# Kernel optimization log

Hardware: AMD Instinct MI355X
Metric: run time of the kernel (lower is better)

## Reference

```python
import jax, jax.numpy as jnp
import numpy as np

N = 50000
E = 1600000
D_IN = 128
D_OUT = 128


def setup_inputs() -> dict:
    key = jax.random.key(0)
    k1, k2, k3, k4, k5, k6 = jax.random.split(key, 6)
    row = jax.random.randint(k1, (E,), 0, N, dtype=jnp.int32)
    col = jax.random.randint(k2, (E,), 0, N, dtype=jnp.int32)
    vals = jax.random.uniform(k3, (E,), dtype=jnp.float32)
    features = jax.random.normal(k4, (N, D_IN), dtype=jnp.float32)
    weight = jax.random.normal(k5, (D_IN, D_OUT), dtype=jnp.float32)
    bias = jax.random.normal(k6, (D_OUT,), dtype=jnp.float32)
    return {"row": row, "col": col, "vals": vals, "features": features,
            "weight": weight, "bias": bias}


def reference(row, col, vals, features, weight, bias):
    # SpMM aggregation: out[i] = sum_j adj[i,j] * features[j]
    # adj given in COO: (row, col, vals)
    gathered = vals[:, None] * features[col]          # [E, D_IN]
    agg = jax.ops.segment_sum(gathered, row, num_segments=N)  # [N, D_IN]
    # dense feature transform + bias
    return agg @ weight + bias                        # [N, D_OUT]
```

## Files before the change

kernel.cpp:

```cpp
#include <hip/hip_runtime.h>
#include <hip/hip_bf16.h>


#define D 128
#define NREP 8
#define RPB 128
#define BCAP 5120
#define EPB 4096
#define NBMAX 512

typedef __attribute__((ext_vector_type(8))) short short8;
typedef __attribute__((ext_vector_type(4))) float f32x4;

__device__ __forceinline__ ushort bf16bits(float x) {
    return __hip_bfloat16_raw(__float2bfloat16(x)).x;
}

__global__ __launch_bounds__(256) void prep_k(const float* __restrict__ W,
                                              ushort* __restrict__ Wt,
                                              int* __restrict__ gcur, int NB) {
    const int idx = blockIdx.x * 256 + threadIdx.x;
    if (idx < D * D) {
        const int k = idx >> 7, c = idx & 127;
        Wt[c * D + k] = bf16bits(W[idx]);
    }
    if (idx < NB) gcur[idx] = 0;
}

__global__ __launch_bounds__(256) void fused_gemm_scatter_k(
    const float* __restrict__ F, const ushort* __restrict__ Wt,
    ushort* __restrict__ Gb, int nrows,
    const int* __restrict__ row, const int* __restrict__ col,
    const float* __restrict__ vals, int* __restrict__ gcur,
    uint2* __restrict__ pairs, int E, int NB, int SB) {
    __shared__ int hist[NBMAX];
    __shared__ int cur[NBMAX];

    if ((int)blockIdx.x >= SB) {
        const int gb = (int)blockIdx.x - SB;
        const int wave = threadIdx.x >> 6;
        const int lane = threadIdx.x & 63;
        const int r0 = (gb * 8 + wave * 2) * 16;
        if (r0 >= nrows) return;
        const int lr = lane & 15;
        const int lg = lane >> 4;

        f32x4 acc0[8], acc1[8];
        #pragma unroll
        for (int c = 0; c < 8; ++c) {
            acc0[c] = (f32x4){0.f, 0.f, 0.f, 0.f};
            acc1[c] = (f32x4){0.f, 0.f, 0.f, 0.f};
        }

        int ar0 = r0 + lr;      if (ar0 >= nrows) ar0 = nrows - 1;
        int ar1 = r0 + 16 + lr; if (ar1 >= nrows) ar1 = nrows - 1;
        const float* __restrict__ a0p = F + (size_t)ar0 * D + lg * 8;
        const float* __restrict__ a1p = F + (size_t)ar1 * D + lg * 8;

        #pragma unroll
        for (int kk = 0; kk < 4; ++kk) {
            const float4 x0 = *(const float4*)(a0p + kk * 32);
            const float4 x1 = *(const float4*)(a0p + kk * 32 + 4);
            const float4 y0 = *(const float4*)(a1p + kk * 32);
            const float4 y1 = *(const float4*)(a1p + kk * 32 + 4);
            short8 af0, af1;
            af0[0] = (short)bf16bits(x0.x); af0[1] = (short)bf16bits(x0.y);
            af0[2] = (short)bf16bits(x0.z); af0[3] = (short)bf16bits(x0.w);
            af0[4] = (short)bf16bits(x1.x); af0[5] = (short)bf16bits(x1.y);
            af0[6] = (short)bf16bits(x1.z); af0[7] = (short)bf16bits(x1.w);
            af1[0] = (short)bf16bits(y0.x); af1[1] = (short)bf16bits(y0.y);
            af1[2] = (short)bf16bits(y0.z); af1[3] = (short)bf16bits(y0.w);
            af1[4] = (short)bf16bits(y1.x); af1[5] = (short)bf16bits(y1.y);
            af1[6] = (short)bf16bits(y1.z); af1[7] = (short)bf16bits(y1.w);
            #pragma unroll
            for (int c = 0; c < 8; ++c) {
                const short8 bf = *(const short8*)(Wt + (size_t)(c * 16 + lr) * D + kk * 32 + lg * 8);
                acc0[c] = __builtin_amdgcn_mfma_f32_16x16x32_bf16(af0, bf, acc0[c], 0, 0, 0);
                acc1[c] = __builtin_amdgcn_mfma_f32_16x16x32_bf16(af1, bf, acc1[c], 0, 0, 0);
            }
        }

        uint* __restrict__ g32 = (uint*)Gb;
        #pragma unroll
        for (int i = 0; i < 4; ++i) {
            const int rr0 = r0 + 4 * lg + i;
            if (rr0 < nrows) {
                #pragma unroll
                for (int c = 0; c < 4; ++c)
                    g32[(size_t)rr0 * 64 + c * 16 + lr] =
                        (uint)bf16bits(acc0[c][i]) | ((uint)bf16bits(acc0[c + 4][i]) << 16);
            }
            const int rr1 = r0 + 16 + 4 * lg + i;
            if (rr1 < nrows) {
                #pragma unroll
                for (int c = 0; c < 4; ++c)
                    g32[(size_t)rr1 * 64 + c * 16 + lr] =
                        (uint)bf16bits(acc1[c][i]) | ((uint)bf16bits(acc1[c + 4][i]) << 16);
            }
        }
        return;
    }

    const int t = threadIdx.x;
    for (int i = t; i < NB; i += 256) hist[i] = 0;
    __syncthreads();

    const int e0 = (int)blockIdx.x * EPB;
    const int e1 = min(e0 + EPB, E);

    for (int e = e0 + t; e < e1; e += 512) {
        const int ra = row[e];
        const bool has2 = (e + 256 < e1);
        const int rb = has2 ? row[e + 256] : 0;
        atomicAdd(&hist[ra >> 7], 1);
        if (has2) atomicAdd(&hist[rb >> 7], 1);
    }
    __syncthreads();

    for (int i = t; i < NB; i += 256) {
        const int h = hist[i];
        cur[i] = (h > 0) ? atomicAdd(&gcur[i], h) : 0;
    }
    __syncthreads();

    for (int e = e0 + t; e < e1; e += 512) {
        const int ra = row[e];
        const int ca = col[e];
        const float va = vals[e];
        const bool has2 = (e + 256 < e1);
        int rb = 0, cb = 0;
        float vb = 0.f;
        if (has2) { rb = row[e + 256]; cb = col[e + 256]; vb = vals[e + 256]; }
        const int ba = ra >> 7;
        const int sa = atomicAdd(&cur[ba], 1);
        if (sa < BCAP)
            pairs[(size_t)ba * BCAP + sa] =
                make_uint2(((uint)ca << 16) | bf16bits(va), (uint)(ra & (RPB - 1)));
        if (has2) {
            const int bb = rb >> 7;
            const int sb = atomicAdd(&cur[bb], 1);
            if (sb < BCAP)
                pairs[(size_t)bb * BCAP + sb] =
                    make_uint2(((uint)cb << 16) | bf16bits(vb), (uint)(rb & (RPB - 1)));
        }
    }
}

__global__ __launch_bounds__(1024) void bucket_to_csr_k(
    uint2* __restrict__ bpairs, const int* __restrict__ gcur,
    int* __restrict__ offs, int* __restrict__ counts, int N) {
    __shared__ uint2 ents[BCAP];
    __shared__ int hist[RPB];
    __shared__ int roff[RPB];
    __shared__ int cur[RPB];
    const int t = threadIdx.x, b = blockIdx.x;
    if (t < RPB) hist[t] = 0;
    __syncthreads();

    int cnt = gcur[b];
    if (cnt > BCAP) cnt = BCAP;
    const uint2* __restrict__ in = bpairs + (size_t)b * BCAP;
    for (int j = t; j < cnt; j += 1024) {
        const uint2 e = in[j];
        ents[j] = e;
        atomicAdd(&hist[e.y], 1);
    }
    __syncthreads();

    if (t < RPB) roff[t] = hist[t];
    __syncthreads();
    for (int off = 1; off < RPB; off <<= 1) {
        const int x = (t < RPB && t >= off) ? roff[t - off] : 0;
        __syncthreads();
        if (t < RPB) roff[t] += x;
        __syncthreads();
    }
    if (t < RPB) {
        const int ex = roff[t] - hist[t];
        roff[t] = ex;
        cur[t] = 0;
        const int rg = b * RPB + t;
        if (rg < N) {
            offs[rg] = b * 2 * BCAP + ex;
            counts[rg] = hist[t];
        }
    }
    __syncthreads();

    uint* __restrict__ outv = (uint*)bpairs + (size_t)b * 2 * BCAP;
    for (int j = t; j < cnt; j += 1024) {
        const uint2 e = ents[j];
        const int k = atomicAdd(&cur[e.y], 1);
        outv[roff[e.y] + k] = e.x;
    }
}

__global__ __launch_bounds__(256) void csr_gather_bf16_k(
    const uint* __restrict__ pairs, const int* __restrict__ offs,
    const int* __restrict__ counts, const uint* __restrict__ Gu,
    const float* __restrict__ bias, float* __restrict__ out, int n) {
    const int wid = (blockIdx.x * 256 + threadIdx.x) >> 6;
    if (wid >= n) return;
    const int lane = threadIdx.x & 63;

    float2 acc = make_float2(bias[lane], bias[64 + lane]);
    const int start = offs[wid];
    const int cnt = counts[wid];
    const uint* __restrict__ pp = pairs + start;

    int j = 0;
    for (; j + 15 < cnt; j += 16) {
        uint p[16], g[16];
        #pragma unroll
        for (int k = 0; k < 16; ++k) p[k] = pp[j + k];
        #pragma unroll
        for (int k = 0; k < 16; ++k) g[k] = Gu[(size_t)(p[k] >> 16) * (D / 2) + lane];
        #pragma unroll
        for (int k = 0; k < 16; ++k) {
            const float v = __uint_as_float(p[k] << 16);
            acc.x += v * __uint_as_float(g[k] << 16);
            acc.y += v * __uint_as_float(g[k] & 0xffff0000u);
        }
    }
    for (; j + 3 < cnt; j += 4) {
        uint p[4], g[4];
        #pragma unroll
        for (int k = 0; k < 4; ++k) p[k] = pp[j + k];
        #pragma unroll
        for (int k = 0; k < 4; ++k) g[k] = Gu[(size_t)(p[k] >> 16) * (D / 2) + lane];
        #pragma unroll
        for (int k = 0; k < 4; ++k) {
            const float v = __uint_as_float(p[k] << 16);
            acc.x += v * __uint_as_float(g[k] << 16);
            acc.y += v * __uint_as_float(g[k] & 0xffff0000u);
        }
    }
    for (; j < cnt; ++j) {
        const uint p = pp[j];
        const uint g = Gu[(size_t)(p >> 16) * (D / 2) + lane];
        const float v = __uint_as_float(p << 16);
        acc.x += v * __uint_as_float(g << 16);
        acc.y += v * __uint_as_float(g & 0xffff0000u);
    }
    out[(size_t)wid * D + lane] = acc.x;
    out[(size_t)wid * D + 64 + lane] = acc.y;
}

__global__ __launch_bounds__(256) void transposeW_k(const float* __restrict__ W,
                                                    ushort* __restrict__ Wt) {
    const int idx = blockIdx.x * 256 + threadIdx.x;
    const int k = idx >> 7, c = idx & 127;
    Wt[c * D + k] = bf16bits(W[idx]);
}

__global__ __launch_bounds__(256) void gemm_mfma_k(
    const float* __restrict__ F, const ushort* __restrict__ Wt,
    ushort* __restrict__ Gb, int nrows) {
    const int wave = threadIdx.x >> 6;
    const int lane = threadIdx.x & 63;
    const int row0 = (blockIdx.x * 4 + wave) * 16;
    if (row0 >= nrows) return;
    const int lr = lane & 15;
    const int lg = lane >> 4;

    f32x4 acc[8];
    #pragma unroll
    for (int c = 0; c < 8; ++c) acc[c] = (f32x4){0.f, 0.f, 0.f, 0.f};

    int arow_idx = row0 + lr;
    if (arow_idx >= nrows) arow_idx = nrows - 1;
    const float* __restrict__ arow = F + (size_t)arow_idx * D + lg * 8;

    #pragma unroll
    for (int kk = 0; kk < 4; ++kk) {
        const float4 a0 = *(const float4*)(arow + kk * 32);
        const float4 a1 = *(const float4*)(arow + kk * 32 + 4);
        short8 af;
        af[0] = (short)bf16bits(a0.x); af[1] = (short)bf16bits(a0.y);
        af[2] = (short)bf16bits(a0.z); af[3] = (short)bf16bits(a0.w);
        af[4] = (short)bf16bits(a1.x); af[5] = (short)bf16bits(a1.y);
        af[6] = (short)bf16bits(a1.z); af[7] = (short)bf16bits(a1.w);
        #pragma unroll
        for (int c = 0; c < 8; ++c) {
            const short8 bf = *(const short8*)(Wt + (size_t)(c * 16 + lr) * D + kk * 32 + lg * 8);
            acc[c] = __builtin_amdgcn_mfma_f32_16x16x32_bf16(af, bf, acc[c], 0, 0, 0);
        }
    }

    ushort* __restrict__ gout = Gb + (size_t)row0 * D;
    #pragma unroll
    for (int i = 0; i < 4; ++i) {
        const int r = 4 * lg + i;
        if (row0 + r < nrows) {
            #pragma unroll
            for (int c = 0; c < 8; ++c) {
                const int j = c * 16 + lr;
                const int pos = (c < 4) ? (2 * j) : (2 * (j - 64) + 1);
                gout[(size_t)r * D + pos] = bf16bits(acc[c][i]);
            }
        }
    }
}

__global__ __launch_bounds__(256) void hist_rank_rep_k(const int* __restrict__ row,
                                                       int* __restrict__ cntrep,
                                                       ushort* __restrict__ rank,
                                                       int E, int N) {
    const int e = blockIdx.x * 256 + threadIdx.x;
    if (e >= E) return;
    const int rep = blockIdx.x & (NREP - 1);
    rank[e] = (ushort)atomicAdd(&cntrep[rep * N + row[e]], 1);
}

__global__ __launch_bounds__(256) void repbase_k(int* __restrict__ cntrep,
                                                 int* __restrict__ tot, int N) {
    const int r = blockIdx.x * 256 + threadIdx.x;
    if (r >= N) return;
    int s = 0;
    #pragma unroll
    for (int rep = 0; rep < NREP; ++rep) {
        const int v = cntrep[rep * N + r];
        cntrep[rep * N + r] = s;
        s += v;
    }
    tot[r] = s;
}

__global__ __launch_bounds__(256) void scan_blocks_k(const int* __restrict__ counts,
                                                     int* __restrict__ offs,
                                                     int* __restrict__ blockSums, int n) {
    __shared__ int s[256];
    const int t = threadIdx.x;
    const int i = blockIdx.x * 256 + t;
    const int v = (i < n) ? counts[i] : 0;
    s[t] = v;
    __syncthreads();
    for (int off = 1; off < 256; off <<= 1) {
        int x = (t >= off) ? s[t - off] : 0;
        __syncthreads();
        s[t] += x;
        __syncthreads();
    }
    if (i < n) offs[i] = s[t] - v;
    if (t == 255) blockSums[blockIdx.x] = s[255];
}

__global__ __launch_bounds__(256) void scan_top_k(int* __restrict__ blockSums, int nb) {
    __shared__ int s[256];
    const int t = threadIdx.x;
    const int v = (t < nb) ? blockSums[t] : 0;
    s[t] = v;
    __syncthreads();
    for (int off = 1; off < 256; off <<= 1) {
        int x = (t >= off) ? s[t - off] : 0;
        __syncthreads();
        s[t] += x;
        __syncthreads();
    }
    if (t < nb) blockSums[t] = s[t] - v;
}

__global__ __launch_bounds__(256) void scan_add_k(int* __restrict__ offs,
                                                  const int* __restrict__ blockSums,
                                                  int n) {
    int i = blockIdx.x * 256 + threadIdx.x;
    if (i < n) offs[i] += blockSums[blockIdx.x];
}

__global__ __launch_bounds__(256) void fill_pack_k(const int* __restrict__ row,
                                                   const int* __restrict__ col,
                                                   const float* __restrict__ vals,
                                                   const int* __restrict__ offs,
                                                   const ushort* __restrict__ rank,
                                                   const int* __restrict__ cntrep,
                                                   uint* __restrict__ pairs, int E, int N) {
    const int e = blockIdx.x * 256 + threadIdx.x;
    if (e >= E) return;
    const int r = row[e];
    const int rep = (e >> 8) & (NREP - 1);
    const int pos = offs[r] + cntrep[rep * N + r] + (int)rank[e];
    pairs[pos] = ((uint)col[e] << 16) | bf16bits(vals[e]);
}

#define ROWS_PER_BLOCK 64
__global__ __launch_bounds__(256) void gemm_f32_k(
    const float* __restrict__ A, const float* __restrict__ W,
    const float* __restrict__ bias, float* __restrict__ out, int nrows) {
    __shared__ float Wlds[D * D];
    {
        const float4* W4 = (const float4*)W;
        float4* Wl4 = (float4*)Wlds;
        #pragma unroll
        for (int i = 0; i < (D * D / 4) / 256; ++i)
            Wl4[threadIdx.x + i * 256] = W4[threadIdx.x + i * 256];
    }
    __syncthreads();
    const int lane = threadIdx.x & 31;
    const int rsub = threadIdx.x >> 5;
    const float4 b = ((const float4*)bias)[lane];
    const int rowBase = blockIdx.x * ROWS_PER_BLOCK;
    for (int rr = rsub; rr < ROWS_PER_BLOCK; rr += 8) {
        const int r = rowBase + rr;
        if (r >= nrows) break;
        const float* __restrict__ arow = A + (size_t)r * D;
        float4 acc = b;
        #pragma unroll 4
        for (int k4 = 0; k4 < D / 4; ++k4) {
            const float4 a = ((const float4*)arow)[k4];
            const int k = k4 * 4;
            const float4 w0 = ((const float4*)(Wlds + (k + 0) * D))[lane];
            const float4 w1 = ((const float4*)(Wlds + (k + 1) * D))[lane];
            const float4 w2 = ((const float4*)(Wlds + (k + 2) * D))[lane];
            const float4 w3 = ((const float4*)(Wlds + (k + 3) * D))[lane];
            acc.x += a.x * w0.x + a.y * w1.x + a.z * w2.x + a.w * w3.x;
            acc.y += a.x * w0.y + a.y * w1.y + a.z * w2.y + a.w * w3.y;
            acc.z += a.x * w0.z + a.y * w1.z + a.z * w2.z + a.w * w3.z;
            acc.w += a.x * w0.w + a.y * w1.w + a.z * w2.w + a.w * w3.w;
        }
        ((float4*)(out + (size_t)r * D))[lane] = acc;
    }
}

__global__ __launch_bounds__(256) void spmm_scatter(
    const int* __restrict__ row, const int* __restrict__ col,
    const float* __restrict__ vals, const float* __restrict__ feat,
    float* __restrict__ agg, int E) {
    int gid = blockIdx.x * 256 + threadIdx.x;
    int e = gid >> 5;
    if (e >= E) return;
    int lane = gid & 31;
    int r = row[e];
    int c = col[e];
    float v = vals[e];
    float4 f = ((const float4*)(feat + (size_t)c * D))[lane];
    float* dst = agg + (size_t)r * D + lane * 4;
    atomicAdd(dst + 0, v * f.x);
    atomicAdd(dst + 1, v * f.y);
    atomicAdd(dst + 2, v * f.z);
    atomicAdd(dst + 3, v * f.w);
}

extern "C" void kernel_launch(void* const* d_in, const int* in_sizes, int n_in,
                              void* d_out, int out_size, void* d_ws, size_t ws_size,
                              hipStream_t stream) {
    const int* row = (const int*)d_in[0];
    const int* col = (const int*)d_in[1];
    const float* vals = (const float*)d_in[2];
    const float* feat = (const float*)d_in[3];
    const float* W = (const float*)d_in[4];
    const float* bias = (const float*)d_in[5];
    float* out = (float*)d_out;

    const int E = in_sizes[0];
    const int N = out_size / D;
    const int NB = (N + RPB - 1) / RPB;

    const size_t Gb_bytes = (size_t)N * D * sizeof(ushort);
    const size_t wt_bytes = (size_t)D * D * sizeof(ushort);
    const size_t cnt_bytes = (size_t)N * sizeof(int);

    const size_t bpairs_bytes = (size_t)NB * BCAP * sizeof(uint2);
    const size_t gcur_bytes = ((size_t)NB * sizeof(int) + 255) & ~(size_t)255;
    const size_t need_bucket = Gb_bytes + bpairs_bytes + gcur_bytes +
                               2 * cnt_bytes + wt_bytes;

    const size_t pairs_bytes = (size_t)E * sizeof(uint);
    const size_t rank_bytes = ((size_t)E * sizeof(ushort) + 3) & ~(size_t)3;
    const size_t cntrep_bytes = (size_t)NREP * N * sizeof(int);
    const size_t bs_bytes = 256 * sizeof(int);
    const size_t need_compact = Gb_bytes + pairs_bytes + rank_bytes + cntrep_bytes +
                                2 * cnt_bytes + bs_bytes + wt_bytes;

    if (ws_size >= need_bucket && N <= 65536 && NB <= NBMAX) {
        char* p = (char*)d_ws;
        ushort* Gb = (ushort*)p;   p += Gb_bytes;
        uint2* bpairs = (uint2*)p; p += bpairs_bytes;
        int* gcur = (int*)p;       p += gcur_bytes;
        int* offs = (int*)p;       p += cnt_bytes;
        int* counts = (int*)p;     p += cnt_bytes;
        ushort* Wt = (ushort*)p;   p += wt_bytes;

        const int GB = (N + 127) / 128;
        const int SB = (E + EPB - 1) / EPB;

        prep_k<<<(D * D + 255) / 256, 256, 0, stream>>>(W, Wt, gcur, NB);
        fused_gemm_scatter_k<<<SB + GB, 256, 0, stream>>>(
            feat, Wt, Gb, N, row, col, vals, gcur, bpairs, E, NB, SB);
        bucket_to_csr_k<<<NB, 1024, 0, stream>>>(bpairs, gcur, offs, counts, N);
        csr_gather_bf16_k<<<(N * 64 + 255) / 256, 256, 0, stream>>>(
            (const uint*)bpairs, offs, counts, (const uint*)Gb, bias, out, N);
    } else if (ws_size >= need_compact && N <= 65536) {
        char* p = (char*)d_ws;
        ushort* Gb = (ushort*)p;   p += Gb_bytes;
        uint* pairs = (uint*)p;    p += pairs_bytes;
        ushort* rank = (ushort*)p; p += rank_bytes;
        int* cntrep = (int*)p;     p += cntrep_bytes;
        int* tot = (int*)p;        p += cnt_bytes;
        int* offs = (int*)p;       p += cnt_bytes;
        int* blockSums = (int*)p;  p += bs_bytes;
        ushort* Wt = (ushort*)p;   p += wt_bytes;

        const int nScanBlocks = (N + 255) / 256;

        transposeW_k<<<(D * D) / 256, 256, 0, stream>>>(W, Wt);
        gemm_mfma_k<<<(N + 63) / 64, 256, 0, stream>>>(feat, Wt, Gb, N);

        hipMemsetAsync(cntrep, 0, cntrep_bytes, stream);
        hist_rank_rep_k<<<(E + 255) / 256, 256, 0, stream>>>(row, cntrep, rank, E, N);
        repbase_k<<<(N + 255) / 256, 256, 0, stream>>>(cntrep, tot, N);
        scan_blocks_k<<<nScanBlocks, 256, 0, stream>>>(tot, offs, blockSums, N);
        scan_top_k<<<1, 256, 0, stream>>>(blockSums, nScanBlocks);
        scan_add_k<<<nScanBlocks, 256, 0, stream>>>(offs, blockSums, N);
        fill_pack_k<<<(E + 255) / 256, 256, 0, stream>>>(row, col, vals, offs, rank,
                                                         cntrep, pairs, E, N);
        csr_gather_bf16_k<<<(N * 64 + 255) / 256, 256, 0, stream>>>(
            pairs, offs, tot, (const uint*)Gb, bias, out, N);
    } else {
        float* agg = (float*)d_ws;
        hipMemsetAsync(agg, 0, (size_t)N * D * sizeof(float), stream);
        long long threads = (long long)E * 32;
        spmm_scatter<<<(int)((threads + 255) / 256), 256, 0, stream>>>(
            row, col, vals, feat, agg, E);
        gemm_f32_k<<<(N + ROWS_PER_BLOCK - 1) / ROWS_PER_BLOCK, 256, 0, stream>>>(
            agg, W, bias, out, N);
    }
}
```

Before: 195.8 us.

## Fuse bucket-to-CSR sort with gather into one per-bucket kernel

Merges the bucket-to-CSR kernel and the gather kernel into a single kernel. Each 1024-thread block sorts its bucket's pairs into LDS and then gathers feature rows for its 128 rows directly, with each wave handling 8 rows. This removes the global write and re-read of the CSR pairs and offsets and one kernel launch. The cost is lower parallelism: about 391 blocks with 16 waves each, each wave processing 8 rows serially, which may reduce the memory-level parallelism available for the random gathers.

```diff
diff --git a/kernel.cpp b/kernel.cpp
--- a/kernel.cpp
+++ b/kernel.cpp
@@ -146,10 +146,11 @@
     }
 }
 
-__global__ __launch_bounds__(1024) void bucket_to_csr_k(
-    uint2* __restrict__ bpairs, const int* __restrict__ gcur,
-    int* __restrict__ offs, int* __restrict__ counts, int N) {
-    __shared__ uint2 ents[BCAP];
+__global__ __launch_bounds__(1024) void csr_fused_k(
+    const uint2* __restrict__ bpairs, const int* __restrict__ gcur,
+    const uint* __restrict__ Gu, const float* __restrict__ bias,
+    float* __restrict__ out, int N) {
+    __shared__ uint lpairs[BCAP];
     __shared__ int hist[RPB];
     __shared__ int roff[RPB];
     __shared__ int cur[RPB];
@@ -160,10 +161,13 @@
     int cnt = gcur[b];
     if (cnt > BCAP) cnt = BCAP;
     const uint2* __restrict__ in = bpairs + (size_t)b * BCAP;
+
+    uint2 ent[5];
+    int ne = 0;
     for (int j = t; j < cnt; j += 1024) {
-        const uint2 e = in[j];
-        ents[j] = e;
-        atomicAdd(&hist[e.y], 1);
+        ent[ne] = in[j];
+        atomicAdd(&hist[ent[ne].y], 1);
+        ++ne;
     }
     __syncthreads();
 
@@ -176,74 +180,67 @@
         __syncthreads();
     }
     if (t < RPB) {
-        const int ex = roff[t] - hist[t];
-        roff[t] = ex;
+        roff[t] -= hist[t];
         cur[t] = 0;
-        const int rg = b * RPB + t;
-        if (rg < N) {
-            offs[rg] = b * 2 * BCAP + ex;
-            counts[rg] = hist[t];
-        }
-    }
-    __syncthreads();
-
-    uint* __restrict__ outv = (uint*)bpairs + (size_t)b * 2 * BCAP;
-    for (int j = t; j < cnt; j += 1024) {
-        const uint2 e = ents[j];
-        const int k = atomicAdd(&cur[e.y], 1);
-        outv[roff[e.y] + k] = e.x;
-    }
-}
-
-__global__ __launch_bounds__(256) void csr_gather_bf16_k(
-    const uint* __restrict__ pairs, const int* __restrict__ offs,
-    const int* __restrict__ counts, const uint* __restrict__ Gu,
-    const float* __restrict__ bias, float* __restrict__ out, int n) {
-    const int wid = (blockIdx.x * 256 + threadIdx.x) >> 6;
-    if (wid >= n) return;
-    const int lane = threadIdx.x & 63;
-
-    float2 acc = make_float2(bias[lane], bias[64 + lane]);
-    const int start = offs[wid];
-    const int cnt = counts[wid];
-    const uint* __restrict__ pp = pairs + start;
-
-    int j = 0;
-    for (; j + 15 < cnt; j += 16) {
-        uint p[16], g[16];
-        #pragma unroll
-        for (int k = 0; k < 16; ++k) p[k] = pp[j + k];
-        #pragma unroll
-        for (int k = 0; k < 16; ++k) g[k] = Gu[(size_t)(p[k] >> 16) * (D / 2) + lane];
-        #pragma unroll
-        for (int k = 0; k < 16; ++k) {
-            const float v = __uint_as_float(p[k] << 16);
-            acc.x += v * __uint_as_float(g[k] << 16);
-            acc.y += v * __uint_as_float(g[k] & 0xffff0000u);
-        }
-    }
-    for (; j + 3 < cnt; j += 4) {
-        uint p[4], g[4];
-        #pragma unroll
-        for (int k = 0; k < 4; ++k) p[k] = pp[j + k];
-        #pragma unroll
-        for (int k = 0; k < 4; ++k) g[k] = Gu[(size_t)(p[k] >> 16) * (D / 2) + lane];
-        #pragma unroll
-        for (int k = 0; k < 4; ++k) {
-            const float v = __uint_as_float(p[k] << 16);
-            acc.x += v * __uint_as_float(g[k] << 16);
-            acc.y += v * __uint_as_float(g[k] & 0xffff0000u);
-        }
-    }
-    for (; j < cnt; ++j) {
-        const uint p = pp[j];
-        const uint g = Gu[(size_t)(p >> 16) * (D / 2) + lane];
-        const float v = __uint_as_float(p << 16);
-        acc.x += v * __uint_as_float(g << 16);
-        acc.y += v * __uint_as_float(g & 0xffff0000u);
-    }
-    out[(size_t)wid * D + lane] = acc.x;
-    out[(size_t)wid * D + 64 + lane] = acc.y;
+    }
+    __syncthreads();
+
+    #pragma unroll
+    for (int k = 0; k < 5; ++k) {
+        if (k < ne) {
+            const int rl = (int)ent[k].y;
+            const int pos = roff[rl] + atomicAdd(&cur[rl], 1);
+            lpairs[pos] = ent[k].x;
+        }
+    }
+    __syncthreads();
+
+    const int wave = t >> 6, lane = t & 63;
+    const float bx = bias[lane], by = bias[64 + lane];
+    for (int rr = wave * 8; rr < wave * 8 + 8; ++rr) {
+        const int r = b * RPB + rr;
+        if (r >= N) continue;
+        float2 acc = make_float2(bx, by);
+        const int cntr = hist[rr];
+        const int base = roff[rr];
+
+        int j = 0;
+        for (; j + 15 < cntr; j += 16) {
+            uint p[16], g[16];
+            #pragma unroll
+            for (int k = 0; k < 16; ++k) p[k] = lpairs[base + j + k];
+            #pragma unroll
+            for (int k = 0; k < 16; ++k) g[k] = Gu[(size_t)(p[k] >> 16) * (D / 2) + lane];
+            #pragma unroll
+            for (int k = 0; k < 16; ++k) {
+                const float v = __uint_as_float(p[k] << 16);
+                acc.x += v * __uint_as_float(g[k] << 16);
+                acc.y += v * __uint_as_float(g[k] & 0xffff0000u);
+            }
+        }
+        for (; j + 3 < cntr; j += 4) {
+            uint p[4], g[4];
+            #pragma unroll
+            for (int k = 0; k < 4; ++k) p[k] = lpairs[base + j + k];
+            #pragma unroll
+            for (int k = 0; k < 4; ++k) g[k] = Gu[(size_t)(p[k] >> 16) * (D / 2) + lane];
+            #pragma unroll
+            for (int k = 0; k < 4; ++k) {
+                const float v = __uint_as_float(p[k] << 16);
+                acc.x += v * __uint_as_float(g[k] << 16);
+                acc.y += v * __uint_as_float(g[k] & 0xffff0000u);
+            }
+        }
+        for (; j < cntr; ++j) {
+            const uint p = lpairs[base + j];
+            const uint g = Gu[(size_t)(p >> 16) * (D / 2) + lane];
+            const float v = __uint_as_float(p << 16);
+            acc.x += v * __uint_as_float(g << 16);
+            acc.y += v * __uint_as_float(g & 0xffff0000u);
+        }
+        out[(size_t)r * D + lane] = acc.x;
+        out[(size_t)r * D + 64 + lane] = acc.y;
+    }
 }
 
 __global__ __launch_bounds__(256) void transposeW_k(const float* __restrict__ W,
@@ -380,6 +377,57 @@
     const int rep = (e >> 8) & (NREP - 1);
     const int pos = offs[r] + cntrep[rep * N + r] + (int)rank[e];
     pairs[pos] = ((uint)col[e] << 16) | bf16bits(vals[e]);
+}
+
+__global__ __launch_bounds__(256) void csr_gather_bf16_k(
+    const uint* __restrict__ pairs, const int* __restrict__ offs,
+    const int* __restrict__ counts, const uint* __restrict__ Gu,
+    const float* __restrict__ bias, float* __restrict__ out, int n) {
+    const int wid = (blockIdx.x * 256 + threadIdx.x) >> 6;
+    if (wid >= n) return;
+    const int lane = threadIdx.x & 63;
+
+    float2 acc = make_float2(bias[lane], bias[64 + lane]);
+    const int start = offs[wid];
+    const int cnt = counts[wid];
+    const uint* __restrict__ pp = pairs + start;
+
+    int j = 0;
+    for (; j + 15 < cnt; j += 16) {
+        uint p[16], g[16];
+        #pragma unroll
+        for (int k = 0; k < 16; ++k) p[k] = pp[j + k];
+        #pragma unroll
+        for (int k = 0; k < 16; ++k) g[k] = Gu[(size_t)(p[k] >> 16) * (D / 2) + lane];
+        #pragma unroll
+        for (int k = 0; k < 16; ++k) {
+            const float v = __uint_as_float(p[k] << 16);
+            acc.x += v * __uint_as_float(g[k] << 16);
+            acc.y += v * __uint_as_float(g[k] & 0xffff0000u);
+        }
+    }
+    for (; j + 3 < cnt; j += 4) {
+        uint p[4], g[4];
+        #pragma unroll
+        for (int k = 0; k < 4; ++k) p[k] = pp[j + k];
+        #pragma unroll
+        for (int k = 0; k < 4; ++k) g[k] = Gu[(size_t)(p[k] >> 16) * (D / 2) + lane];
+        #pragma unroll
+        for (int k = 0; k < 4; ++k) {
+            const float v = __uint_as_float(p[k] << 16);
+            acc.x += v * __uint_as_float(g[k] << 16);
+            acc.y += v * __uint_as_float(g[k] & 0xffff0000u);
+        }
+    }
+    for (; j < cnt; ++j) {
+        const uint p = pp[j];
+        const uint g = Gu[(size_t)(p >> 16) * (D / 2) + lane];
+        const float v = __uint_as_float(p << 16);
+        acc.x += v * __uint_as_float(g << 16);
+        acc.y += v * __uint_as_float(g & 0xffff0000u);
+    }
+    out[(size_t)wid * D + lane] = acc.x;
+    out[(size_t)wid * D + 64 + lane] = acc.y;
 }
 
 #define ROWS_PER_BLOCK 64
@@ -461,8 +509,7 @@
 
     const size_t bpairs_bytes = (size_t)NB * BCAP * sizeof(uint2);
     const size_t gcur_bytes = ((size_t)NB * sizeof(int) + 255) & ~(size_t)255;
-    const size_t need_bucket = Gb_bytes + bpairs_bytes + gcur_bytes +
-                               2 * cnt_bytes + wt_bytes;
+    const size_t need_bucket = Gb_bytes + bpairs_bytes + gcur_bytes + wt_bytes;
 
     const size_t pairs_bytes = (size_t)E * sizeof(uint);
     const size_t rank_bytes = ((size_t)E * sizeof(ushort) + 3) & ~(size_t)3;
@@ -476,8 +523,6 @@
         ushort* Gb = (ushort*)p;   p += Gb_bytes;
         uint2* bpairs = (uint2*)p; p += bpairs_bytes;
         int* gcur = (int*)p;       p += gcur_bytes;
-        int* offs = (int*)p;       p += cnt_bytes;
-        int* counts = (int*)p;     p += cnt_bytes;
         ushort* Wt = (ushort*)p;   p += wt_bytes;
 
         const int GB = (N + 127) / 128;
@@ -486,9 +531,8 @@
         prep_k<<<(D * D + 255) / 256, 256, 0, stream>>>(W, Wt, gcur, NB);
         fused_gemm_scatter_k<<<SB + GB, 256, 0, stream>>>(
             feat, Wt, Gb, N, row, col, vals, gcur, bpairs, E, NB, SB);
-        bucket_to_csr_k<<<NB, 1024, 0, stream>>>(bpairs, gcur, offs, counts, N);
-        csr_gather_bf16_k<<<(N * 64 + 255) / 256, 256, 0, stream>>>(
-            (const uint*)bpairs, offs, counts, (const uint*)Gb, bias, out, N);
+        csr_fused_k<<<NB, 1024, 0, stream>>>(bpairs, gcur, (const uint*)Gb, bias,
+                                             out, N);
     } else if (ws_size >= need_compact && N <= 65536) {
         char* p = (char*)d_ws;
         ushort* Gb = (ushort*)p;   p += Gb_bytes;
```

After: 198.0 us. No clear change (+1.1%).
